# Kernel optimization log

Measured on AMD Instinct MI355X. Metric: run time of the kernel, lower is better.

The kernel has to match this reference:

```python
import jax, jax.numpy as jnp
import numpy as np

D_MODEL = 1024
N_HEADS = 16
HEAD_DIM = D_MODEL // N_HEADS
B, L = 2, 2048


def setup_inputs() -> dict:
    key = jax.random.key(0)
    ks = jax.random.split(key, 9)
    s = 1.0 / np.sqrt(D_MODEL)
    return {
        "hidden_states": jax.random.normal(ks[0], (B, L, D_MODEL), dtype=jnp.float32),
        "Wq": jax.random.uniform(ks[1], (D_MODEL, D_MODEL), jnp.float32, -s, s),
        "bq": jax.random.uniform(ks[2], (D_MODEL,), jnp.float32, -s, s),
        "Wk": jax.random.uniform(ks[3], (D_MODEL, D_MODEL), jnp.float32, -s, s),
        "bk": jax.random.uniform(ks[4], (D_MODEL,), jnp.float32, -s, s),
        "Wv": jax.random.uniform(ks[5], (D_MODEL, D_MODEL), jnp.float32, -s, s),
        "bv": jax.random.uniform(ks[6], (D_MODEL,), jnp.float32, -s, s),
        "Wo": jax.random.uniform(ks[7], (D_MODEL, D_MODEL), jnp.float32, -s, s),
        "bo": jax.random.uniform(ks[8], (D_MODEL,), jnp.float32, -s, s),
    }


def reference(hidden_states, Wq, bq, Wk, bk, Wv, bv, Wo, bo):
    b, l, d = hidden_states.shape
    h, hd = N_HEADS, HEAD_DIM
    scale = jnp.sqrt(jnp.asarray(hd, hidden_states.dtype))
    # projections (weights stored as [in, out], equivalent to torch Linear W.T)
    Q = (hidden_states @ Wq + bq).reshape(b, l, h, hd).transpose(0, 2, 1, 3)
    K = (hidden_states @ Wk + bk).reshape(b, l, h, hd).transpose(0, 2, 1, 3)
    V = (hidden_states @ Wv + bv).reshape(b, l, h, hd).transpose(0, 2, 1, 3)
    # [b, h, l, l] scores with causal mask
    scores = jnp.einsum("bhqd,bhkd->bhqk", Q, K) / scale
    causal = jnp.tril(jnp.ones((l, l), dtype=bool))
    scores = jnp.where(causal, scores, jnp.asarray(-jnp.inf, scores.dtype))
    weights = jax.nn.softmax(scores, axis=-1)
    out = jnp.einsum("bhqk,bhkd->bhqd", weights, V)
    out = out.transpose(0, 2, 1, 3).reshape(b, l, d)
    return out @ Wo + bo
```

## Files before the change

kernel.cpp:

```cpp
#include <hip/hip_runtime.h>

typedef unsigned short u16;
typedef unsigned int u32;
typedef __attribute__((ext_vector_type(8))) short bf16x8;
typedef __attribute__((ext_vector_type(4))) float f32x4;

__device__ __forceinline__ u16 f2bf(float f) {
    union { float f; u32 u; } x; x.f = f;
    u32 r = x.u + 0x7FFFu + ((x.u >> 16) & 1u);
    return (u16)(r >> 16);
}

__device__ __forceinline__ u16 f2bf_fast(float f) {
    union { float f; u32 u; } x; x.f = f;
    return (u16)((x.u + 0x8000u) >> 16);
}

__device__ __forceinline__ void gload16(const u16* g, u16* l) {
    __builtin_amdgcn_global_load_lds(
        (const __attribute__((address_space(1))) void*)g,
        (__attribute__((address_space(3))) void*)l,
        16, 0, 0);
}

__device__ __forceinline__ f32x4 mfma16(bf16x8 a, bf16x8 b, f32x4 c) {
    return __builtin_amdgcn_mfma_f32_16x16x32_bf16(a, b, c, 0, 0, 0);
}


__global__ __launch_bounds__(256) void cvt_x(const float* __restrict__ in, u16* __restrict__ out, int n4) {
    int i = blockIdx.x * blockDim.x + threadIdx.x;
    if (i >= n4) return;
    float4 v = ((const float4*)in)[i];
    u16* o = out + (size_t)i * 4;
    o[0] = f2bf(v.x); o[1] = f2bf(v.y); o[2] = f2bf(v.z); o[3] = f2bf(v.w);
}

__global__ __launch_bounds__(256) void transpose_w4(const float* __restrict__ Wq, const float* __restrict__ Wk,
                                                    const float* __restrict__ Wv, const float* __restrict__ Wo,
                                                    const float* __restrict__ bq, const float* __restrict__ bk,
                                                    const float* __restrict__ bv,
                                                    u16* __restrict__ qkvt, u16* __restrict__ wot,
                                                    float* __restrict__ bqkv) {
    __shared__ float tile[32][33];
    const float* in;
    u16* out;
    if (blockIdx.z == 0)      { in = Wq; out = qkvt; }
    else if (blockIdx.z == 1) { in = Wk; out = qkvt + 1024 * 1024; }
    else if (blockIdx.z == 2) { in = Wv; out = qkvt + 2 * 1024 * 1024; }
    else                      { in = Wo; out = wot; }
    if (blockIdx.z == 3 && blockIdx.x == 0 && blockIdx.y == 0) {
        for (int i = threadIdx.x; i < 3072; i += 256)
            bqkv[i] = (i < 1024) ? bq[i] : ((i < 2048) ? bk[i - 1024] : bv[i - 2048]);
    }
    const int bx = blockIdx.x * 32, by = blockIdx.y * 32;
    const int tx = threadIdx.x & 31, ty4 = (threadIdx.x >> 5) * 4;
#pragma unroll
    for (int j = 0; j < 4; ++j)
        tile[ty4 + j][tx] = in[(size_t)(by + ty4 + j) * 1024 + bx + tx];
    __syncthreads();
#pragma unroll
    for (int j = 0; j < 4; ++j)
        out[(size_t)(bx + ty4 + j) * 1024 + by + tx] = f2bf(tile[tx][ty4 + j]);
}

template<int MODE>
__global__ __launch_bounds__(256) void gemm128(const u16* __restrict__ A, const u16* __restrict__ Bt,
                                               const float* __restrict__ bias,
                                               u16* __restrict__ oq, u16* __restrict__ ok, u16* __restrict__ ov,
                                               float* __restrict__ of, int K)
{
    __shared__ u16 As[128 * 64];
    __shared__ u16 Bs[128 * 64];

    const int NB = (MODE == 0) ? 24 : 8;
    const int CHUNK = (MODE == 0) ? 96 : 32;
    const int f = (int)blockIdx.x;
    const int g2 = (f & 7) * CHUNK + (f >> 3);
    const int n0 = (g2 % NB) * 128;
    const int m0 = (g2 / NB) * 128;

    const int t = threadIdx.x;
    const int w = t >> 6, lane = t & 63;
    const int g = lane >> 4, lr = lane & 15;
    const int wm = w >> 1, wn = w & 1;
    const int sw = lr & 7;

    const int srow = lane >> 3;
    const int schunk = (lane & 7) ^ srow;
    const u16* pA = A  + (size_t)(m0 + w * 8 + srow) * K + schunk * 8;
    const u16* pB = Bt + (size_t)(n0 + w * 8 + srow) * K + schunk * 8;
    u16* lA = &As[w * 512 + lane * 8];
    u16* lB = &Bs[w * 512 + lane * 8];

    const int sa_row = (wm * 64 + lr) * 64;
    const int sb_row = (wn * 64 + lr) * 64;

    f32x4 acc[4][4] = {};

    for (int k0 = 0; k0 < K; k0 += 64) {
        __syncthreads();
#pragma unroll
        for (int i = 0; i < 4; ++i) {
            gload16(pA + (size_t)i * 32 * K + k0, lA + i * 2048);
            gload16(pB + (size_t)i * 32 * K + k0, lB + i * 2048);
        }
        __syncthreads();
#pragma unroll
        for (int kk = 0; kk < 2; ++kk) {
            const int cofs = ((kk * 4 + g) ^ sw) * 8;
            bf16x8 af[4], bf[4];
#pragma unroll
            for (int mi = 0; mi < 4; ++mi) af[mi] = *(const bf16x8*)&As[sa_row + mi * 16 * 64 + cofs];
#pragma unroll
            for (int ni = 0; ni < 4; ++ni) bf[ni] = *(const bf16x8*)&Bs[sb_row + ni * 16 * 64 + cofs];
#pragma unroll
            for (int mi = 0; mi < 4; ++mi)
#pragma unroll
                for (int ni = 0; ni < 4; ++ni)
                    acc[mi][ni] = mfma16(af[mi], bf[ni], acc[mi][ni]);
        }
    }

#pragma unroll
    for (int mi = 0; mi < 4; ++mi) {
#pragma unroll
        for (int ni = 0; ni < 4; ++ni) {
            const int col = n0 + wn * 64 + ni * 16 + lr;
            const int row0 = m0 + wm * 64 + mi * 16 + g * 4;
            const float bs = bias[col];
            if (MODE == 0) {
                const int mat = col >> 10;
                const int nn = col & 1023;
                const int h = nn >> 6, d = nn & 63;
                const int b = row0 >> 11, ll0 = row0 & 2047;
                const int bh = b * 16 + h;
                if (mat == 0) {
#pragma unroll
                    for (int j = 0; j < 4; ++j)
                        oq[((size_t)bh * 2048 + ll0 + j) * 64 + d] =
                            f2bf((acc[mi][ni][j] + bs) * 0.1803368801111244f);
                } else if (mat == 1) {
#pragma unroll
                    for (int j = 0; j < 4; ++j)
                        ok[((size_t)bh * 2048 + ll0 + j) * 64 + d] = f2bf(acc[mi][ni][j] + bs);
                } else {
                    union { ushort4 s4; u16 u[4]; } pk;
#pragma unroll
                    for (int j = 0; j < 4; ++j) pk.u[j] = f2bf(acc[mi][ni][j] + bs);
                    *(ushort4*)&ov[((size_t)bh * 64 + d) * 2048 + ll0] = pk.s4;
                }
            } else {
#pragma unroll
                for (int j = 0; j < 4; ++j)
                    of[(size_t)(row0 + j) * 1024 + col] = acc[mi][ni][j] + bs;
            }
        }
    }
}

__global__ __launch_bounds__(256) void attn(const u16* __restrict__ Q, const u16* __restrict__ Kg,
                                            const u16* __restrict__ Vt, u16* __restrict__ O,
                                            float* __restrict__ Opart, float* __restrict__ Mp,
                                            float* __restrict__ Lp, int do_split)
{
    __shared__ u16 Ks[64 * 64];
    __shared__ u16 Vs[64 * 64];
    __shared__ u16 Ps[4][16 * 64];

    const int bh = blockIdx.x;
    int qb, k_lo, k_hi, split;
    if (!do_split) {
        qb = 31 - (int)blockIdx.y; k_lo = 0; k_hi = qb + 1; split = -1;
    } else {
        const int y = (int)blockIdx.y;
        if (y < 32) {
            qb = 16 + (y >> 1);
            split = y & 1;
            const int mid = (qb + 1) >> 1;
            k_lo = split ? mid : 0;
            k_hi = split ? qb + 1 : mid;
        } else {
            qb = 47 - y; k_lo = 0; k_hi = qb + 1; split = -1;
        }
    }
    const int q0 = qb * 64;
    const int t = threadIdx.x;
    const int w = t >> 6, lane = t & 63;
    const int g = lane >> 4, lr = lane & 15;
    const int qw = q0 + w * 16;
    const int sw = lr & 7;

    const u16* Qb = Q  + (size_t)bh * 2048 * 64;
    const u16* Kb = Kg + (size_t)bh * 2048 * 64;
    const u16* Vb = Vt + (size_t)bh * 64 * 2048;

    const bf16x8 qf0 = *(const bf16x8*)&Qb[(size_t)(qw + lr) * 64 + g * 8];
    const bf16x8 qf1 = *(const bf16x8*)&Qb[(size_t)(qw + lr) * 64 + 32 + g * 8];

    const short one = (short)0x3F80;
    const bf16x8 vones = {one, one, one, one, one, one, one, one};

    f32x4 oacc[4] = {};
    f32x4 lsacc = {};
    float mrun = -1e30f;

    int bpaddr[4];
#pragma unroll
    for (int j = 0; j < 4; ++j) bpaddr[j] = (20 * g + j) * 4;

    const int pw_base = lr * 64;
    const int g2h = g >> 1;
    const int wic2 = (2 * g) & 3;

    bf16x8 kreg[2], vreg[2];
    const int srow0 = t >> 3, sch = t & 7;
    auto issue = [&](int kb) {
#pragma unroll
        for (int i = 0; i < 2; ++i) {
            const int row = srow0 + i * 32;
            kreg[i] = *(const bf16x8*)&Kb[(size_t)(kb * 64 + row) * 64 + sch * 8];
            vreg[i] = *(const bf16x8*)&Vb[(size_t)row * 2048 + kb * 64 + sch * 8];
        }
    };
    auto commit = [&]() {
#pragma unroll
        for (int i = 0; i < 2; ++i) {
            const int row = srow0 + i * 32;
            const int chs = sch ^ (row & 7);
            *(bf16x8*)&Ks[row * 64 + chs * 8] = kreg[i];
            *(bf16x8*)&Vs[row * 64 + chs * 8] = vreg[i];
        }
    };

    issue(k_lo);

    for (int kb = k_lo; kb < k_hi; ++kb) {
        const int k0 = kb * 64;
        __syncthreads();
        commit();
        __syncthreads();
        if (kb + 1 < k_hi) issue(kb + 1);

        f32x4 s[4] = {};
        __builtin_amdgcn_s_setprio(1);
#pragma unroll
        for (int ni = 0; ni < 4; ++ni) {
            const int row = ni * 16 + lr;
            bf16x8 kf0 = *(const bf16x8*)&Ks[row * 64 + (g ^ sw) * 8];
            bf16x8 kf1 = *(const bf16x8*)&Ks[row * 64 + ((4 + g) ^ sw) * 8];
            s[ni] = mfma16(kf0, qf0, s[ni]);
            s[ni] = mfma16(kf1, qf1, s[ni]);
        }
        __builtin_amdgcn_s_setprio(0);

        if (kb == qb) {
            const int qq = qw + lr;
#pragma unroll
            for (int ni = 0; ni < 4; ++ni)
#pragma unroll
                for (int j = 0; j < 4; ++j)
                    if (k0 + ni * 16 + g * 4 + j > qq) s[ni][j] = -1e30f;
        }

        float pm = fmaxf(fmaxf(fmaxf(s[0][0], s[0][1]), fmaxf(s[0][2], s[0][3])),
                         fmaxf(fmaxf(s[1][0], s[1][1]), fmaxf(s[1][2], s[1][3])));
        pm = fmaxf(pm, fmaxf(fmaxf(fmaxf(s[2][0], s[2][1]), fmaxf(s[2][2], s[2][3])),
                             fmaxf(fmaxf(s[3][0], s[3][1]), fmaxf(s[3][2], s[3][3]))));
        pm = fmaxf(pm, __shfl_xor(pm, 16));
        pm = fmaxf(pm, __shfl_xor(pm, 32));

        if (__any(pm > mrun + 8.f)) {
            const float mn = fmaxf(mrun, pm);
            const float r = __builtin_amdgcn_exp2f(mrun - mn);
            mrun = mn;
            const int ri = __float_as_int(r);
#pragma unroll
            for (int j = 0; j < 4; ++j) {
                const float ro = __int_as_float(__builtin_amdgcn_ds_bpermute(bpaddr[j], ri));
                lsacc[j] *= ro;
#pragma unroll
                for (int df = 0; df < 4; ++df) oacc[df][j] *= ro;
            }
        }

#pragma unroll
        for (int ni = 0; ni < 4; ++ni) {
            const int c8 = 2 * ni + g2h;
#pragma unroll
            for (int jp = 0; jp < 2; ++jp) {
                const float plo = __builtin_amdgcn_exp2f(s[ni][2 * jp]     - mrun);
                const float phi = __builtin_amdgcn_exp2f(s[ni][2 * jp + 1] - mrun);
                const u32 pr = (u32)f2bf_fast(plo) | ((u32)f2bf_fast(phi) << 16);
                const int wic = wic2 + jp;
                *(u32*)&Ps[w][pw_base + (c8 ^ sw) * 8 + wic * 2] = pr;
            }
        }

        const bf16x8 p0 = *(const bf16x8*)&Ps[w][lr * 64 + (g ^ sw) * 8];
        const bf16x8 p1 = *(const bf16x8*)&Ps[w][lr * 64 + ((4 + g) ^ sw) * 8];
        __builtin_amdgcn_s_setprio(1);
        lsacc = mfma16(p0, vones, lsacc);
        lsacc = mfma16(p1, vones, lsacc);
#pragma unroll
        for (int df = 0; df < 4; ++df) {
            const int row = df * 16 + lr;
            bf16x8 vf0 = *(const bf16x8*)&Vs[row * 64 + (g ^ sw) * 8];
            bf16x8 vf1 = *(const bf16x8*)&Vs[row * 64 + ((4 + g) ^ sw) * 8];
            oacc[df] = mfma16(p0, vf0, oacc[df]);
            oacc[df] = mfma16(p1, vf1, oacc[df]);
        }
        __builtin_amdgcn_s_setprio(0);
    }

    if (split < 0) {
        const int b = bh >> 4, h = bh & 15;
#pragma unroll
        for (int j = 0; j < 4; ++j) {
            const float inv = 1.f / lsacc[j];
            const int l = qw + g * 4 + j;
#pragma unroll
            for (int df = 0; df < 4; ++df)
                O[((size_t)b * 2048 + l) * 1024 + h * 64 + df * 16 + lr] = f2bf(oacc[df][j] * inv);
        }
    } else {
        float* Ob = Opart + ((size_t)split * 32 + bh) * (1024 * 64);
        const int rb = qw - 1024 + 4 * g;
#pragma unroll
        for (int j = 0; j < 4; ++j)
#pragma unroll
            for (int df = 0; df < 4; ++df)
                Ob[(size_t)(rb + j) * 64 + df * 16 + lr] = oacc[df][j];
        if (lr == 0) {
#pragma unroll
            for (int j = 0; j < 4; ++j)
                Lp[(split * 32 + bh) * 1024 + rb + j] = lsacc[j];
        }
        if (g == 0)
            Mp[(split * 32 + bh) * 1024 + (qw - 1024) + lr] = mrun;
    }
}

__global__ __launch_bounds__(256) void attn_merge(const float* __restrict__ Opart,
                                                  const float* __restrict__ Mp,
                                                  const float* __restrict__ Lp,
                                                  u16* __restrict__ O)
{
    const int idx = blockIdx.x * 256 + threadIdx.x;
    const int d  = idx & 63;
    const int rr = (idx >> 6) & 1023;
    const int bh = idx >> 16;
    const int si = bh * 1024 + rr;
    const float m0 = Mp[si], m1 = Mp[32 * 1024 + si];
    const float l0 = Lp[si], l1 = Lp[32 * 1024 + si];
    const float M  = fmaxf(m0, m1);
    const float w0 = __builtin_amdgcn_exp2f(m0 - M);
    const float w1 = __builtin_amdgcn_exp2f(m1 - M);
    const float o0 = Opart[(size_t)si * 64 + d];
    const float o1 = Opart[(size_t)(32 * 1024 + si) * 64 + d];
    const float o  = (w0 * o0 + w1 * o1) / (w0 * l0 + w1 * l1);
    const int b = bh >> 4, h = bh & 15;
    const int r = 1024 + rr;
    O[((size_t)b * 2048 + r) * 1024 + h * 64 + d] = f2bf(o);
}


extern "C" void kernel_launch(void* const* d_in, const int* in_sizes, int n_in,
                              void* d_out, int out_size, void* d_ws, size_t ws_size,
                              hipStream_t stream)
{
    const float* hs = (const float*)d_in[0];
    const float* Wq = (const float*)d_in[1];
    const float* bq = (const float*)d_in[2];
    const float* Wk = (const float*)d_in[3];
    const float* bk = (const float*)d_in[4];
    const float* Wv = (const float*)d_in[5];
    const float* bv = (const float*)d_in[6];
    const float* Wo = (const float*)d_in[7];
    const float* bo = (const float*)d_in[8];
    float* out = (float*)d_out;

    char* ws = (char*)d_ws;
    u16*   Xbf   = (u16*)(ws);
    u16*   Wqkvt = (u16*)(ws + (8ull  << 20));
    u16*   Wot   = (u16*)(ws + (14ull << 20));
    float* bqkv  = (float*)(ws + (16ull << 20));
    u16*   Qbuf  = (u16*)(ws + (17ull << 20));
    u16*   Kbuf  = (u16*)(ws + (25ull << 20));
    u16*   Vtbuf = (u16*)(ws + (33ull << 20));
    u16*   Abuf  = Xbf;
    float* Opart = (float*)(ws + (42ull << 20));
    float* Mpart = (float*)(ws + (58ull << 20));
    float* Lpart = (float*)(ws + (58ull << 20) + (512ull << 10));

    const int do_split = (ws_size >= (59ull << 20)) ? 1 : 0;

    cvt_x<<<4096, 256, 0, stream>>>(hs, Xbf, 4096 * 1024 / 4);
    transpose_w4<<<dim3(32, 32, 4), 256, 0, stream>>>(Wq, Wk, Wv, Wo, bq, bk, bv, Wqkvt, Wot, bqkv);

    gemm128<0><<<768, 256, 0, stream>>>(Xbf, Wqkvt, bqkv, Qbuf, Kbuf, Vtbuf, nullptr, 1024);

    if (do_split) {
        attn<<<dim3(32, 48), 256, 0, stream>>>(Qbuf, Kbuf, Vtbuf, Abuf, Opart, Mpart, Lpart, 1);
        attn_merge<<<8192, 256, 0, stream>>>(Opart, Mpart, Lpart, Abuf);
    } else {
        attn<<<dim3(32, 32), 256, 0, stream>>>(Qbuf, Kbuf, Vtbuf, Abuf, nullptr, nullptr, nullptr, 0);
    }

    gemm128<1><<<256, 256, 0, stream>>>(Abuf, Wot, bo, nullptr, nullptr, nullptr, out, 1024);
}
```

Before: 123.7 us.

## Add 64x128-tile output-projection GEMM and store split-attention partials as bf16

Replaces the shared 128x128 GEMM template for the output projection with a dedicated 64x128-tile kernel on an 8x64 grid, so 512 blocks instead of 256 fill the device's compute units. The split-attention partial outputs are now normalized per split and stored as bf16 rather than fp32, halving partial-buffer traffic, and the merge kernel reweights them by exp(m)*l. The QKV GEMM becomes a non-templated copy. The trade is lower data reuse per block in the output GEMM and reduced precision in the partial sums.

Measured after the change: 122.3 us. No clear change (-1.2%).

```diff
diff --git a/kernel.cpp b/kernel.cpp
--- a/kernel.cpp
+++ b/kernel.cpp
@@ -14,6 +14,10 @@
 __device__ __forceinline__ u16 f2bf_fast(float f) {
     union { float f; u32 u; } x; x.f = f;
     return (u16)((x.u + 0x8000u) >> 16);
+}
+
+__device__ __forceinline__ float bf2f(u16 v) {
+    union { u32 u; float f; } x; x.u = (u32)v << 16; return x.f;
 }
 
 __device__ __forceinline__ void gload16(const u16* g, u16* l) {
@@ -64,17 +68,15 @@
         out[(size_t)(bx + ty4 + j) * 1024 + by + tx] = f2bf(tile[tx][ty4 + j]);
 }
 
-template<int MODE>
-__global__ __launch_bounds__(256) void gemm128(const u16* __restrict__ A, const u16* __restrict__ Bt,
-                                               const float* __restrict__ bias,
-                                               u16* __restrict__ oq, u16* __restrict__ ok, u16* __restrict__ ov,
-                                               float* __restrict__ of, int K)
+__global__ __launch_bounds__(256) void gemm128_qkv(const u16* __restrict__ A, const u16* __restrict__ Bt,
+                                                   const float* __restrict__ bias,
+                                                   u16* __restrict__ oq, u16* __restrict__ ok, u16* __restrict__ ov)
 {
     __shared__ u16 As[128 * 64];
     __shared__ u16 Bs[128 * 64];
 
-    const int NB = (MODE == 0) ? 24 : 8;
-    const int CHUNK = (MODE == 0) ? 96 : 32;
+    const int K = 1024;
+    const int NB = 24, CHUNK = 96;
     const int f = (int)blockIdx.x;
     const int g2 = (f & 7) * CHUNK + (f >> 3);
     const int n0 = (g2 % NB) * 128;
@@ -129,39 +131,95 @@
             const int col = n0 + wn * 64 + ni * 16 + lr;
             const int row0 = m0 + wm * 64 + mi * 16 + g * 4;
             const float bs = bias[col];
-            if (MODE == 0) {
-                const int mat = col >> 10;
-                const int nn = col & 1023;
-                const int h = nn >> 6, d = nn & 63;
-                const int b = row0 >> 11, ll0 = row0 & 2047;
-                const int bh = b * 16 + h;
-                if (mat == 0) {
-#pragma unroll
-                    for (int j = 0; j < 4; ++j)
-                        oq[((size_t)bh * 2048 + ll0 + j) * 64 + d] =
-                            f2bf((acc[mi][ni][j] + bs) * 0.1803368801111244f);
-                } else if (mat == 1) {
-#pragma unroll
-                    for (int j = 0; j < 4; ++j)
-                        ok[((size_t)bh * 2048 + ll0 + j) * 64 + d] = f2bf(acc[mi][ni][j] + bs);
-                } else {
-                    union { ushort4 s4; u16 u[4]; } pk;
-#pragma unroll
-                    for (int j = 0; j < 4; ++j) pk.u[j] = f2bf(acc[mi][ni][j] + bs);
-                    *(ushort4*)&ov[((size_t)bh * 64 + d) * 2048 + ll0] = pk.s4;
-                }
+            const int mat = col >> 10;
+            const int nn = col & 1023;
+            const int h = nn >> 6, d = nn & 63;
+            const int b = row0 >> 11, ll0 = row0 & 2047;
+            const int bh = b * 16 + h;
+            if (mat == 0) {
+#pragma unroll
+                for (int j = 0; j < 4; ++j)
+                    oq[((size_t)bh * 2048 + ll0 + j) * 64 + d] =
+                        f2bf((acc[mi][ni][j] + bs) * 0.1803368801111244f);
+            } else if (mat == 1) {
+#pragma unroll
+                for (int j = 0; j < 4; ++j)
+                    ok[((size_t)bh * 2048 + ll0 + j) * 64 + d] = f2bf(acc[mi][ni][j] + bs);
             } else {
-#pragma unroll
-                for (int j = 0; j < 4; ++j)
-                    of[(size_t)(row0 + j) * 1024 + col] = acc[mi][ni][j] + bs;
+                union { ushort4 s4; u16 u[4]; } pk;
+#pragma unroll
+                for (int j = 0; j < 4; ++j) pk.u[j] = f2bf(acc[mi][ni][j] + bs);
+                *(ushort4*)&ov[((size_t)bh * 64 + d) * 2048 + ll0] = pk.s4;
             }
         }
     }
+}
+
+__global__ __launch_bounds__(256) void gemm_o(const u16* __restrict__ A, const u16* __restrict__ Bt,
+                                              const float* __restrict__ bias, float* __restrict__ of)
+{
+    __shared__ u16 As[64 * 64];
+    __shared__ u16 Bs[128 * 64];
+
+    const int K = 1024;
+    const int n0 = blockIdx.x * 128;
+    const int m0 = blockIdx.y * 64;
+    const int t = threadIdx.x;
+    const int w = t >> 6, lane = t & 63;
+    const int g = lane >> 4, lr = lane & 15;
+    const int sw = lr & 7;
+    const int wn = w;
+
+    const int srow8 = t >> 3;
+    const int sch = t & 7;
+    const int schunk = sch ^ (srow8 & 7);
+    const u16* pA = A  + (size_t)(m0 + srow8) * K + schunk * 8;
+    const u16* pB = Bt + (size_t)(n0 + srow8) * K + schunk * 8;
+    const int ldst = srow8 * 64 + sch * 8;
+
+    f32x4 acc[4][2] = {};
+
+    for (int k0 = 0; k0 < K; k0 += 64) {
+        __syncthreads();
+#pragma unroll
+        for (int i = 0; i < 2; ++i)
+            gload16(pA + (size_t)(i * 32) * K + k0, &As[i * 2048 + ldst]);
+#pragma unroll
+        for (int i = 0; i < 4; ++i)
+            gload16(pB + (size_t)(i * 32) * K + k0, &Bs[i * 2048 + ldst]);
+        __syncthreads();
+#pragma unroll
+        for (int kk = 0; kk < 2; ++kk) {
+            const int cofs = ((kk * 4 + g) ^ sw) * 8;
+            bf16x8 af[4], bf[2];
+#pragma unroll
+            for (int mi = 0; mi < 4; ++mi) af[mi] = *(const bf16x8*)&As[(mi * 16 + lr) * 64 + cofs];
+#pragma unroll
+            for (int ni = 0; ni < 2; ++ni) bf[ni] = *(const bf16x8*)&Bs[(wn * 32 + ni * 16 + lr) * 64 + cofs];
+#pragma unroll
+            for (int mi = 0; mi < 4; ++mi)
+#pragma unroll
+                for (int ni = 0; ni < 2; ++ni)
+                    acc[mi][ni] = mfma16(af[mi], bf[ni], acc[mi][ni]);
+        }
+    }
+
+#pragma unroll
+    for (int mi = 0; mi < 4; ++mi)
+#pragma unroll
+        for (int ni = 0; ni < 2; ++ni) {
+            const int col = n0 + wn * 32 + ni * 16 + lr;
+            const int row0 = m0 + mi * 16 + g * 4;
+            const float bs = bias[col];
+#pragma unroll
+            for (int j = 0; j < 4; ++j)
+                of[(size_t)(row0 + j) * 1024 + col] = acc[mi][ni][j] + bs;
+        }
 }
 
 __global__ __launch_bounds__(256) void attn(const u16* __restrict__ Q, const u16* __restrict__ Kg,
                                             const u16* __restrict__ Vt, u16* __restrict__ O,
-                                            float* __restrict__ Opart, float* __restrict__ Mp,
+                                            u16* __restrict__ Opart, float* __restrict__ Mp,
                                             float* __restrict__ Lp, int do_split)
 {
     __shared__ u16 Ks[64 * 64];
@@ -324,24 +382,22 @@
                 O[((size_t)b * 2048 + l) * 1024 + h * 64 + df * 16 + lr] = f2bf(oacc[df][j] * inv);
         }
     } else {
-        float* Ob = Opart + ((size_t)split * 32 + bh) * (1024 * 64);
+        u16* Ob = Opart + ((size_t)split * 32 + bh) * (1024 * 64);
         const int rb = qw - 1024 + 4 * g;
 #pragma unroll
-        for (int j = 0; j < 4; ++j)
+        for (int j = 0; j < 4; ++j) {
+            const float inv = 1.f / lsacc[j];
 #pragma unroll
             for (int df = 0; df < 4; ++df)
-                Ob[(size_t)(rb + j) * 64 + df * 16 + lr] = oacc[df][j];
-        if (lr == 0) {
-#pragma unroll
-            for (int j = 0; j < 4; ++j)
-                Lp[(split * 32 + bh) * 1024 + rb + j] = lsacc[j];
+                Ob[(size_t)(rb + j) * 64 + df * 16 + lr] = f2bf(oacc[df][j] * inv);
+            if (lr == 0) Lp[(split * 32 + bh) * 1024 + rb + j] = lsacc[j];
         }
         if (g == 0)
             Mp[(split * 32 + bh) * 1024 + (qw - 1024) + lr] = mrun;
     }
 }
 
-__global__ __launch_bounds__(256) void attn_merge(const float* __restrict__ Opart,
+__global__ __launch_bounds__(256) void attn_merge(const u16* __restrict__ Opart,
                                                   const float* __restrict__ Mp,
                                                   const float* __restrict__ Lp,
                                                   u16* __restrict__ O)
@@ -354,11 +410,11 @@
     const float m0 = Mp[si], m1 = Mp[32 * 1024 + si];
     const float l0 = Lp[si], l1 = Lp[32 * 1024 + si];
     const float M  = fmaxf(m0, m1);
-    const float w0 = __builtin_amdgcn_exp2f(m0 - M);
-    const float w1 = __builtin_amdgcn_exp2f(m1 - M);
-    const float o0 = Opart[(size_t)si * 64 + d];
-    const float o1 = Opart[(size_t)(32 * 1024 + si) * 64 + d];
-    const float o  = (w0 * o0 + w1 * o1) / (w0 * l0 + w1 * l1);
+    const float v0 = __builtin_amdgcn_exp2f(m0 - M) * l0;
+    const float v1 = __builtin_amdgcn_exp2f(m1 - M) * l1;
+    const float o0 = bf2f(Opart[(size_t)si * 64 + d]);
+    const float o1 = bf2f(Opart[(size_t)(32 * 1024 + si) * 64 + d]);
+    const float o  = (v0 * o0 + v1 * o1) / (v0 + v1);
     const int b = bh >> 4, h = bh & 15;
     const int r = 1024 + rr;
     O[((size_t)b * 2048 + r) * 1024 + h * 64 + d] = f2bf(o);
@@ -389,7 +445,7 @@
     u16*   Kbuf  = (u16*)(ws + (25ull << 20));
     u16*   Vtbuf = (u16*)(ws + (33ull << 20));
     u16*   Abuf  = Xbf;
-    float* Opart = (float*)(ws + (42ull << 20));
+    u16*   Opart = (u16*)(ws + (42ull << 20));
     float* Mpart = (float*)(ws + (58ull << 20));
     float* Lpart = (float*)(ws + (58ull << 20) + (512ull << 10));
 
@@ -398,7 +454,7 @@
     cvt_x<<<4096, 256, 0, stream>>>(hs, Xbf, 4096 * 1024 / 4);
     transpose_w4<<<dim3(32, 32, 4), 256, 0, stream>>>(Wq, Wk, Wv, Wo, bq, bk, bv, Wqkvt, Wot, bqkv);
 
-    gemm128<0><<<768, 256, 0, stream>>>(Xbf, Wqkvt, bqkv, Qbuf, Kbuf, Vtbuf, nullptr, 1024);
+    gemm128_qkv<<<768, 256, 0, stream>>>(Xbf, Wqkvt, bqkv, Qbuf, Kbuf, Vtbuf);
 
     if (do_split) {
         attn<<<dim3(32, 48), 256, 0, stream>>>(Qbuf, Kbuf, Vtbuf, Abuf, Opart, Mpart, Lpart, 1);
@@ -407,5 +463,5 @@
         attn<<<dim3(32, 32), 256, 0, stream>>>(Qbuf, Kbuf, Vtbuf, Abuf, nullptr, nullptr, nullptr, 0);
     }
 
-    gemm128<1><<<256, 256, 0, stream>>>(Abuf, Wot, bo, nullptr, nullptr, nullptr, out, 1024);
-}
+    gemm_o<<<dim3(8, 64), 256, 0, stream>>>(Abuf, Wot, bo, out);
+}
```
